# Kernel optimization log

Measured on AMD Instinct MI355X. Metric: run time of the kernel, lower is better.

## Reference

```python
import jax, jax.numpy as jnp
import numpy as np

H = 8          # num_heads
DM = 128       # dmodel
BN_EPS = 1e-5


def _linear(x, w, b):
    # w stored as [in, out]
    return x @ w + b


def _relu_mha(q, k, v, qw, qb, kw, kb, vw, vb, ow, ob, mask):
    """TemMulHeadAtte: ReLU on projected Q/K/V, masked softmax, ReLU out-proj.
    q,k: [B,N,T,2*DM]; v: [B,N,T,DM]; mask: broadcastable to [B,N,H,T,T] or None."""
    B, N, T, _ = q.shape
    Q = jax.nn.relu(_linear(q, qw, qb)).reshape(B, N, T, H, -1)  # e = 2*DM/H
    K = jax.nn.relu(_linear(k, kw, kb)).reshape(B, N, T, H, -1)
    V = jax.nn.relu(_linear(v, vw, vb)).reshape(B, N, T, H, -1)  # d = DM/H
    scale = 1.0 / np.sqrt(Q.shape[-1]).astype(np.float32)
    scores = jnp.einsum('bnthe,bnshe->bnhts', Q, K)
    if mask is not None:
        scores = jnp.where(mask, -jnp.inf, scores)
    attn = jax.nn.softmax(scale * scores, axis=-1)  # dropout p=0 -> identity
    out = jnp.einsum('bnhts,bnshd->bnthd', attn, V).reshape(B, N, T, -1)
    return jax.nn.relu(_linear(out, ow, ob))


def setup_inputs() -> dict:
    key = jax.random.key(0)
    ks = iter(jax.random.split(key, 32))
    B, N, T = 16, 207, 24
    def w(shape, scale=0.05):
        return (jax.random.normal(next(ks), shape, dtype=jnp.float32) * scale)
    inp = {
        'x': w((B, N, T, DM), 1.0),
        'hidden': w((B, N, T, DM), 1.0),
        'tXin': w((B, N, T, DM), 1.0),
    }
    dk = 2 * DM // H * H   # 256
    dv = DM // H * H       # 128
    for pre in ('s', 't'):  # space / temporal attention params
        inp[pre + 'q_w'] = w((2 * DM, dk)); inp[pre + 'q_b'] = w((dk,))
        inp[pre + 'k_w'] = w((2 * DM, dk)); inp[pre + 'k_b'] = w((dk,))
        inp[pre + 'v_w'] = w((DM, dv));     inp[pre + 'v_b'] = w((dv,))
        inp[pre + 'o_w'] = w((dv, DM));     inp[pre + 'o_b'] = w((DM,))
    inp['gate_w'] = w((2 * DM, DM)); inp['gate_b'] = w((DM,))
    inp['bn_gamma'] = jnp.ones((DM,), jnp.float32)
    inp['bn_beta'] = jnp.zeros((DM,), jnp.float32)
    return inp


def reference(x, hidden, tXin,
              sq_w, sq_b, sk_w, sk_b, sv_w, sv_b, so_w, so_b,
              tq_w, tq_b, tk_w, tk_b, tv_w, tv_b, to_w, to_b,
              gate_w, gate_b, bn_gamma, bn_beta):
    B, N, T, E = hidden.shape
    ht = jnp.concatenate([hidden, tXin], axis=3)  # [B,N,T,2*DM]
    # spatial attention: attend over nodes (N<->T permute)
    sqk = ht.transpose(0, 2, 1, 3)        # [B,T,N,2*DM]
    sval = hidden.transpose(0, 2, 1, 3)   # [B,T,N,DM]
    spaceOut = _relu_mha(sqk, sqk, sval, sq_w, sq_b, sk_w, sk_b, sv_w, sv_b,
                         so_w, so_b, None).transpose(0, 2, 1, 3)  # [B,N,T,DM]
    # temporal attention with causal (strict upper-tri) mask
    mask = jnp.triu(jnp.ones((T, T), dtype=bool), 1)[None, None, None]
    tempOut = _relu_mha(ht, ht, hidden, tq_w, tq_b, tk_w, tk_b, tv_w, tv_b,
                        to_w, to_b, mask)  # [B,N,T,DM]
    # gate + BatchNorm2d over channel dim (training-mode batch stats, biased var)
    gi = _linear(jnp.concatenate([spaceOut, tempOut], axis=3), gate_w, gate_b)
    mean = gi.mean(axis=(0, 1, 2))
    var = gi.var(axis=(0, 1, 2))
    z = jax.nn.sigmoid((gi - mean) * jax.lax.rsqrt(var + BN_EPS) * bn_gamma + bn_beta)
    return z * spaceOut + (1.0 - z) * tempOut
```

## Files before the change

kernel.cpp:

```cpp
#include <hip/hip_runtime.h>
#include <hip/hip_bf16.h>

typedef __bf16 bf16;
typedef __bf16 bf16x8 __attribute__((ext_vector_type(8)));
typedef float f32x4 __attribute__((ext_vector_type(4)));

#define MTOT 79488
#define NDIM 207
#define TDIM 24

#define EXP2F(x) __builtin_amdgcn_exp2f(x)

__global__ void detect_dtype(const void* __restrict__ hidden, int* __restrict__ flag)
{
    __shared__ int cnt;
    if (threadIdx.x == 0) cnt = 0;
    __syncthreads();
    const bf16* h = (const bf16*)hidden;
    int local = 0;
    for (int i = threadIdx.x; i < 4096; i += 256) {
        float v = (float)h[i];
        if (!(fabsf(v) < 1e6f)) local++;
    }
    atomicAdd(&cnt, local);
    __syncthreads();
    if (threadIdx.x == 0) *flag = (cnt > 8) ? 1 : 0;
}

__device__ inline float ld_ext(const void* p, int idx, int isF32)
{
    return isF32 ? ((const float*)p)[idx] : (float)((const bf16*)p)[idx];
}

__global__ __launch_bounds__(256) void cvt_inputs(
    const void* __restrict__ hidden, const void* __restrict__ tXin,
    bf16* __restrict__ hb, bf16* __restrict__ tb, const int* __restrict__ dtf)
{
    const int isF32 = *dtf;
    const void* src = blockIdx.y ? tXin : hidden;
    bf16* dst = blockIdx.y ? tb : hb;
    const size_t e8 = ((size_t)blockIdx.x * 256 + threadIdx.x) * 8;
    bf16x8 v;
    if (isF32) {
        f32x4 lo = *(const f32x4*)((const float*)src + e8);
        f32x4 hi = *(const f32x4*)((const float*)src + e8 + 4);
        v[0]=(bf16)lo[0]; v[1]=(bf16)lo[1]; v[2]=(bf16)lo[2]; v[3]=(bf16)lo[3];
        v[4]=(bf16)hi[0]; v[5]=(bf16)hi[1]; v[6]=(bf16)hi[2]; v[7]=(bf16)hi[3];
    } else {
        v = *(const bf16x8*)((const bf16*)src + e8);
    }
    *(bf16x8*)(dst + e8) = v;
}

__global__ __launch_bounds__(256) void prep_weights(
    const void* __restrict__ sq, const void* __restrict__ sk, const void* __restrict__ sv,
    const void* __restrict__ so, const void* __restrict__ tq, const void* __restrict__ tk,
    const void* __restrict__ tv, const void* __restrict__ to_, const void* __restrict__ gw,
    const void* __restrict__ sqb, const void* __restrict__ skb, const void* __restrict__ svb,
    const void* __restrict__ sob, const void* __restrict__ tqb, const void* __restrict__ tkb,
    const void* __restrict__ tvb, const void* __restrict__ tob, const void* __restrict__ gb,
    bf16* __restrict__ wdst, bf16* __restrict__ bdst, const int* __restrict__ dtf)
{
    const int isF32 = *dtf;
    if (blockIdx.x == 1536) {
        for (int j = threadIdx.x; j < 1664; j += 256) {
            const void* src; int i2;
            if      (j < 256)  { src = sqb; i2 = j; }
            else if (j < 512)  { src = skb; i2 = j - 256; }
            else if (j < 640)  { src = svb; i2 = j - 512; }
            else if (j < 896)  { src = tqb; i2 = j - 640; }
            else if (j < 1152) { src = tkb; i2 = j - 896; }
            else if (j < 1280) { src = tvb; i2 = j - 1152; }
            else if (j < 1408) { src = sob; i2 = j - 1280; }
            else if (j < 1536) { src = tob; i2 = j - 1408; }
            else               { src = gb;  i2 = j - 1536; }
            bdst[j] = (bf16)ld_ext(src, i2, isF32);
        }
        return;
    }
    const int e = blockIdx.x * 256 + threadIdx.x;
    float v;
    if (e < 327680) {
        int br = (e >= 163840);
        int e2 = e - br * 163840;
        int n = e2 >> 8, k = e2 & 255;
        const void* qw = br ? tq : sq;
        const void* kw = br ? tk : sk;
        const void* vw = br ? tv : sv;
        if      (n < 256) v = ld_ext(qw, k * 256 + n, isF32);
        else if (n < 512) v = ld_ext(kw, k * 256 + (n - 256), isF32);
        else              v = (k < 128) ? ld_ext(vw, k * 128 + (n - 512), isF32) : 0.f;
    } else if (e < 360448) {
        int br = (e >= 344064);
        int e2 = e - 327680 - br * 16384;
        int n = e2 >> 7, k = e2 & 127;
        v = ld_ext(br ? to_ : so, k * 128 + n, isF32);
    } else {
        int e2 = e - 360448;
        int n = e2 >> 8, k = e2 & 255;
        v = ld_ext(gw, k * 128 + n, isF32);
    }
    wdst[e] = (bf16)v;
}

__global__ __launch_bounds__(256) void gemm_bt(
    const void* __restrict__ A0v, const void* __restrict__ A1v,
    const bf16* __restrict__ Bt, const bf16* __restrict__ bias,
    bf16* __restrict__ C, int Nout, int Ktot, int doRelu, int aExt,
    const int* __restrict__ dtf, int permMode, float* __restrict__ stats, int ntx)
{
    const int aF32 = aExt & *dtf;
    __shared__ bf16 smem[2 * 128 * 72];
    bf16* As = smem;
    bf16* Bs = smem + 128 * 72;
    __shared__ float lsum[128], lsq[128];
    const int tid  = threadIdx.x;
    const int wid  = tid >> 6, lane = tid & 63;
    const int wm   = (wid >> 1) * 64, wn = (wid & 1) * 64;
    const int quad = lane >> 4, l16 = lane & 15;

    int m0, n0;
    {
        const int nwg = (int)gridDim.x;
        const int lid = (int)blockIdx.x;
        const int q = nwg >> 3, r = nwg & 7;
        const int xcd = lid & 7, idx = lid >> 3;
        const int nid = (xcd < r ? xcd * (q + 1) : r * (q + 1) + (xcd - r) * q) + idx;
        m0 = (nid / ntx) * 128;
        n0 = (nid % ntx) * 128;
    }

    const int lrow = tid >> 3;
    const int lcol = (tid & 7) * 8;

    bf16x8 av[4], bv[4];
    auto loadTiles = [&](int k0) {
        const void* Ap = (k0 < 128) ? A0v : A1v;
        const int koff = (k0 < 128) ? k0 : k0 - 128;
        #pragma unroll
        for (int p = 0; p < 4; ++p) {
            int r = lrow + p * 32;
            if (aF32) {
                const float* Af = (const float*)Ap;
                f32x4 lo = *(const f32x4*)(Af + (size_t)(m0 + r) * 128 + koff + lcol);
                f32x4 hi = *(const f32x4*)(Af + (size_t)(m0 + r) * 128 + koff + lcol + 4);
                bf16x8 t;
                t[0]=(bf16)lo[0]; t[1]=(bf16)lo[1]; t[2]=(bf16)lo[2]; t[3]=(bf16)lo[3];
                t[4]=(bf16)hi[0]; t[5]=(bf16)hi[1]; t[6]=(bf16)hi[2]; t[7]=(bf16)hi[3];
                av[p] = t;
            } else {
                av[p] = *(const bf16x8*)((const bf16*)Ap + (size_t)(m0 + r) * 128 + koff + lcol);
            }
            bv[p] = *(const bf16x8*)(Bt + (size_t)(n0 + r) * Ktot + k0 + lcol);
        }
    };

    loadTiles(0);
    f32x4 acc[4][4] = {};

    for (int k0 = 0; k0 < Ktot; k0 += 64) {
        #pragma unroll
        for (int p = 0; p < 4; ++p) {
            int r = lrow + p * 32;
            *(bf16x8*)&As[r * 72 + lcol] = av[p];
            *(bf16x8*)&Bs[r * 72 + lcol] = bv[p];
        }
        __syncthreads();
        if (k0 + 64 < Ktot) loadTiles(k0 + 64);
        #pragma unroll
        for (int kk = 0; kk < 64; kk += 32) {
            bf16x8 af[4], bfr[4];
            #pragma unroll
            for (int i = 0; i < 4; ++i)
                af[i] = *(const bf16x8*)&As[(wm + i * 16 + l16) * 72 + kk + quad * 8];
            #pragma unroll
            for (int j = 0; j < 4; ++j)
                bfr[j] = *(const bf16x8*)&Bs[(wn + j * 16 + l16) * 72 + kk + quad * 8];
            #pragma unroll
            for (int i = 0; i < 4; ++i)
                #pragma unroll
                for (int j = 0; j < 4; ++j)
                    acc[i][j] = __builtin_amdgcn_mfma_f32_16x16x32_bf16(
                        af[i], bfr[j], acc[i][j], 0, 0, 0);
        }
        __syncthreads();
    }

    if (stats) {
        if (tid < 128) { lsum[tid] = 0.f; lsq[tid] = 0.f; }
        __syncthreads();
    }
    #pragma unroll
    for (int j = 0; j < 4; ++j) {
        int col = n0 + wn + j * 16 + l16;
        float bv2 = (float)bias[col];
        float ps = 0.f, psq = 0.f;
        #pragma unroll
        for (int i = 0; i < 4; ++i) {
            #pragma unroll
            for (int r = 0; r < 4; ++r) {
                float v = acc[i][j][r] + bv2;
                if (doRelu) v = fmaxf(v, 0.f);
                if (stats) { ps += v; psq += v * v; }
                acc[i][j][r] = v;
            }
        }
        if (stats) {
            atomicAdd(&lsum[col & 127], ps);
            atomicAdd(&lsq[col & 127], psq);
        }
    }

    bf16* Cs = smem;
    #pragma unroll
    for (int j = 0; j < 4; ++j)
        #pragma unroll
        for (int i = 0; i < 4; ++i)
            #pragma unroll
            for (int r = 0; r < 4; ++r)
                Cs[(wm + i * 16 + quad * 4 + r) * 132 + wn + j * 16 + l16]
                    = (bf16)acc[i][j][r];
    __syncthreads();

    if (stats && tid < 128) {
        atomicAdd(&stats[tid], lsum[tid]);
        atomicAdd(&stats[128 + tid], lsq[tid]);
    }

    const int srow = tid >> 4, scol = (tid & 15) * 8;
    #pragma unroll
    for (int pass = 0; pass < 8; ++pass) {
        int rl = pass * 16 + srow;
        int m = m0 + rl;
        int o;
        if (permMode == 1) {
            int t = m % 24, bn = m / 24;
            int n = bn % 207, b = bn / 207;
            o = (b * 24 + t) * 207 + n;
        } else if (permMode == 2) {
            int n = m % 207, bt = m / 207;
            int t = bt % 24, b = bt / 24;
            o = (b * 207 + n) * 24 + t;
        } else {
            o = m;
        }
        bf16x8 v = *(const bf16x8*)&Cs[rl * 132 + scol];
        *(bf16x8*)&C[(size_t)o * Nout + n0 + scol] = v;
    }
}

__global__ __launch_bounds__(256) void attn_spatial_mfma(
    const bf16* __restrict__ QKV, bf16* __restrict__ O)
{
    const int hh = blockIdx.x, t = blockIdx.y, b = blockIdx.z;
    __shared__ bf16 Ks[208 * 40];
    __shared__ bf16 Vt[16 * 232];
    __shared__ bf16 Pl[4][2][16 * 40];
    const int tid = threadIdx.x;
    const int wave = tid >> 6, lane = tid & 63;
    const int quad = lane >> 4, l16 = lane & 15;
    const size_t R = (size_t)(b * TDIM + t) * NDIM;

    for (int idx = tid; idx < 832; idx += 256) {
        int n = idx >> 2, seg = (idx & 3) * 8;
        bf16x8 v8 = {};
        if (n < NDIM)
            v8 = *(const bf16x8*)(QKV + (R + n) * 640 + 256 + hh * 32 + seg);
        *(bf16x8*)&Ks[n * 40 + seg] = v8;
    }
    for (int idx = tid; idx < 448; idx += 256) {
        int s = idx >> 1, half = (idx & 1) * 8;
        bf16x8 v8 = {};
        if (s < NDIM)
            v8 = *(const bf16x8*)(QKV + (R + s) * 640 + 512 + hh * 16 + half);
        #pragma unroll
        for (int j = 0; j < 8; ++j)
            Vt[(half + j) * 232 + s] = v8[j];
    }
    __syncthreads();

    const float k2 = 0.25506538410868237f;

    for (int qt = wave; qt < 13; qt += 4) {
        const int q0 = qt * 16;
        int qrow = q0 + l16; if (qrow >= NDIM) qrow = NDIM - 1;
        bf16x8 qfrag = *(const bf16x8*)(QKV + (R + qrow) * 640 + hh * 32 + quad * 8);
        f32x4 s[13];
        #pragma unroll
        for (int c = 0; c < 13; ++c) {
            bf16x8 kf = *(const bf16x8*)&Ks[(c * 16 + l16) * 40 + quad * 8];
            f32x4 z = {};
            s[c] = __builtin_amdgcn_mfma_f32_16x16x32_bf16(qfrag, kf, z, 0, 0, 0);
        }
        float linv[4];
        #pragma unroll
        for (int r = 0; r < 4; ++r) {
            float sum = 0.f;
            #pragma unroll
            for (int c = 0; c < 13; ++c) {
                float p = EXP2F(s[c][r] * k2);
                if (c == 12 && l16 == 15) p = 0.f;
                s[c][r] = p;
                sum += p;
            }
            sum += __shfl_xor(sum, 1);
            sum += __shfl_xor(sum, 2);
            sum += __shfl_xor(sum, 4);
            sum += __shfl_xor(sum, 8);
            linv[r] = __builtin_amdgcn_rcpf(sum);
        }
        f32x4 oacc = {};
        #pragma unroll
        for (int sc = 0; sc < 7; ++sc) {
            bf16* pb = &Pl[wave][sc & 1][0];
            #pragma unroll
            for (int r = 0; r < 4; ++r) {
                float p1 = 0.f;
                if (sc < 6) p1 = s[2 * sc + 1][r];
                pb[(quad * 4 + r) * 40 + l16]      = (bf16)s[2 * sc][r];
                pb[(quad * 4 + r) * 40 + 16 + l16] = (bf16)p1;
            }
            bf16x8 pf = *(const bf16x8*)&pb[l16 * 40 + quad * 8];
            bf16x8 vf = *(const bf16x8*)&Vt[l16 * 232 + sc * 32 + quad * 8];
            oacc = __builtin_amdgcn_mfma_f32_16x16x32_bf16(pf, vf, oacc, 0, 0, 0);
        }
        #pragma unroll
        for (int r = 0; r < 4; ++r) {
            int row = q0 + quad * 4 + r;
            if (row < NDIM)
                O[(R + row) * 128 + hh * 16 + l16] = (bf16)(oacc[r] * linv[r]);
        }
    }
}

__global__ __launch_bounds__(256) void attn_temporal_mfma(
    const bf16* __restrict__ QKV, bf16* __restrict__ O)
{
    const size_t m0 = (size_t)blockIdx.x * TDIM;
    __shared__ bf16 Khs[8 * 32 * 40];
    __shared__ bf16 Vts[8 * 16 * 40];
    __shared__ bf16 Pl[4][2][16 * 40];
    const int tid = threadIdx.x;
    const int wave = tid >> 6, lane = tid & 63;
    const int quad = lane >> 4, l16 = lane & 15;
    const int STR = 640;

    for (int idx = tid; idx < 32 * 32; idx += 256) {
        int row = idx >> 5, seg = idx & 31;
        int h = seg >> 2, j = (seg & 3) * 8;
        bf16x8 v8 = {};
        if (row < TDIM)
            v8 = *(const bf16x8*)(QKV + (m0 + row) * STR + 256 + h * 32 + j);
        *(bf16x8*)&Khs[h * 1280 + row * 40 + j] = v8;
    }
    for (int idx = tid; idx < 32 * 128; idx += 256) {
        int s = idx >> 7, c = idx & 127;
        int h = c >> 4, d = c & 15;
        bf16 v = (bf16)0.f;
        if (s < TDIM) v = QKV[(m0 + s) * STR + 512 + h * 16 + d];
        Vts[h * 640 + d * 40 + s] = v;
    }
    __syncthreads();

    const float k2 = 0.25506538410868237f;

    #pragma unroll
    for (int hi = 0; hi < 2; ++hi) {
        const int h = wave * 2 + hi;
        #pragma unroll
        for (int qt = 0; qt < 2; ++qt) {
            int qrow = qt * 16 + l16; if (qrow >= TDIM) qrow = TDIM - 1;
            bf16x8 qfrag = *(const bf16x8*)(QKV + (m0 + qrow) * STR + h * 32 + quad * 8);
            bf16x8 kf0 = *(const bf16x8*)&Khs[h * 1280 + l16 * 40 + quad * 8];
            bf16x8 kf1 = *(const bf16x8*)&Khs[h * 1280 + (16 + l16) * 40 + quad * 8];
            f32x4 z = {};
            f32x4 s0 = __builtin_amdgcn_mfma_f32_16x16x32_bf16(qfrag, kf0, z, 0, 0, 0);
            f32x4 s1 = __builtin_amdgcn_mfma_f32_16x16x32_bf16(qfrag, kf1, z, 0, 0, 0);
            bf16* pb = &Pl[wave][qt][0];
            float linv[4];
            #pragma unroll
            for (int r = 0; r < 4; ++r) {
                int q = qt * 16 + quad * 4 + r;
                float p0 = (l16 <= q)      ? EXP2F(s0[r] * k2) : 0.f;
                float p1 = (16 + l16 <= q) ? EXP2F(s1[r] * k2) : 0.f;
                float sum = p0 + p1;
                sum += __shfl_xor(sum, 1);
                sum += __shfl_xor(sum, 2);
                sum += __shfl_xor(sum, 4);
                sum += __shfl_xor(sum, 8);
                linv[r] = __builtin_amdgcn_rcpf(sum);
                pb[(quad * 4 + r) * 40 + l16]      = (bf16)p0;
                pb[(quad * 4 + r) * 40 + 16 + l16] = (bf16)p1;
            }
            bf16x8 pf = *(const bf16x8*)&pb[l16 * 40 + quad * 8];
            bf16x8 vf = *(const bf16x8*)&Vts[h * 640 + l16 * 40 + quad * 8];
            f32x4 oacc = __builtin_amdgcn_mfma_f32_16x16x32_bf16(pf, vf, z, 0, 0, 0);
            #pragma unroll
            for (int r = 0; r < 4; ++r) {
                int row = qt * 16 + quad * 4 + r;
                if (row < TDIM)
                    O[(m0 + row) * 128 + h * 16 + l16] = (bf16)(oacc[r] * linv[r]);
            }
        }
    }
}

__global__ __launch_bounds__(256) void bn_final(
    const bf16* __restrict__ gi, const bf16* __restrict__ sp, const bf16* __restrict__ tp,
    const void* __restrict__ gammav, const void* __restrict__ betav,
    const float* __restrict__ stats, void* __restrict__ outv,
    const int* __restrict__ dtf)
{
    const int isF32 = *dtf;
    const size_t base = ((size_t)blockIdx.x * 256 + threadIdx.x) * 8;
    const int c0 = (int)(base & 127);
    const float invM = 1.f / (float)MTOT;
    bf16x8 g8 = *(const bf16x8*)(gi + base);
    bf16x8 s8 = *(const bf16x8*)(sp + base);
    bf16x8 t8 = *(const bf16x8*)(tp + base);
    float res[8];
    #pragma unroll
    for (int j = 0; j < 8; ++j) {
        int c = c0 + j;
        float mean = stats[c] * invM;
        float var  = stats[128 + c] * invM - mean * mean;
        float gam = ld_ext(gammav, c, isF32);
        float bet = ld_ext(betav, c, isF32);
        float g = (float)g8[j];
        float zn = (g - mean) * rsqrtf(var + 1e-5f) * gam + bet;
        float z = 1.f / (1.f + EXP2F(zn * -1.4426950408889634f));
        float sv = (float)s8[j], tv = (float)t8[j];
        res[j] = z * sv + (1.f - z) * tv;
    }
    if (isF32) {
        float* op = (float*)outv + base;
        f32x4 lo = {res[0], res[1], res[2], res[3]};
        f32x4 hi = {res[4], res[5], res[6], res[7]};
        *(f32x4*)op = lo;
        *(f32x4*)(op + 4) = hi;
    } else {
        bf16x8 o8;
        #pragma unroll
        for (int j = 0; j < 8; ++j) o8[j] = (bf16)res[j];
        *(bf16x8*)((bf16*)outv + base) = o8;
    }
}

extern "C" void kernel_launch(void* const* d_in, const int* in_sizes, int n_in,
                              void* d_out, int out_size, void* d_ws, size_t ws_size,
                              hipStream_t stream)
{
    const void* hidden = d_in[1];
    const void* tXin   = d_in[2];
    const void* sq_w = d_in[3];  const void* sq_b = d_in[4];
    const void* sk_w = d_in[5];  const void* sk_b = d_in[6];
    const void* sv_w = d_in[7];  const void* sv_b = d_in[8];
    const void* so_w = d_in[9];  const void* so_b = d_in[10];
    const void* tq_w = d_in[11]; const void* tq_b = d_in[12];
    const void* tk_w = d_in[13]; const void* tk_b = d_in[14];
    const void* tv_w = d_in[15]; const void* tv_b = d_in[16];
    const void* to_w = d_in[17]; const void* to_b = d_in[18];
    const void* gate_w = d_in[19]; const void* gate_b = d_in[20];
    const void* gamma  = d_in[21]; const void* beta   = d_in[22];

    char* ws = (char*)d_ws;
    float* stats = (float*)ws;
    int*  dtf    = (int*)(ws + 1024);
    bf16* bB     = (bf16*)(ws + 2048);
    bf16* wT     = (bf16*)(ws + 8192);
    bf16* spaceO = (bf16*)(ws + 794624);
    bf16* attnO  = (bf16*)(ws + 21143552);
    bf16* QKV    = (bf16*)(ws + 41492480);
    bf16* hb     = (bf16*)(ws + 143237120);
    bf16* tb     = (bf16*)(ws + 163586048);
    bf16* tempO  = attnO;
    bf16* gi     = QKV;

    const int wsBig = (ws_size >= 184000000ull);

    bf16* sW  = wT;            bf16* tW  = wT + 163840;
    bf16* soT = wT + 327680;   bf16* toT = wT + 344064;
    bf16* gwT = wT + 360448;

    (void)hipMemsetAsync(stats, 0, 1024, stream);
    detect_dtype<<<1, 256, 0, stream>>>(hidden, dtf);
    prep_weights<<<dim3(1537), 256, 0, stream>>>(
        sq_w, sk_w, sv_w, so_w, tq_w, tk_w, tv_w, to_w, gate_w,
        sq_b, sk_b, sv_b, so_b, tq_b, tk_b, tv_b, to_b, gate_b,
        wT, bB, dtf);
    if (wsBig)
        cvt_inputs<<<dim3(4968, 2), 256, 0, stream>>>(hidden, tXin, hb, tb, dtf);

    const void* A0 = wsBig ? (const void*)hb : hidden;
    const void* A1 = wsBig ? (const void*)tb : tXin;
    const int aExt = wsBig ? 0 : 1;

    gemm_bt<<<dim3(3105), 256, 0, stream>>>(A0, A1, sW, bB, QKV, 640, 256, 1, aExt, dtf, 1, nullptr, 5);
    attn_spatial_mfma<<<dim3(8, TDIM, 16), 256, 0, stream>>>(QKV, attnO);
    gemm_bt<<<dim3(621), 256, 0, stream>>>(attnO, nullptr, soT, bB + 1280, spaceO, 128, 128, 1, 0, dtf, 2, nullptr, 1);

    gemm_bt<<<dim3(3105), 256, 0, stream>>>(A0, A1, tW, bB + 640, QKV, 640, 256, 1, aExt, dtf, 0, nullptr, 5);
    attn_temporal_mfma<<<dim3(16 * NDIM), 256, 0, stream>>>(QKV, attnO);
    gemm_bt<<<dim3(621), 256, 0, stream>>>(attnO, nullptr, toT, bB + 1408, tempO, 128, 128, 1, 0, dtf, 0, nullptr, 1);

    gemm_bt<<<dim3(621), 256, 0, stream>>>(spaceO, tempO, gwT, bB + 1536, gi, 128, 256, 0, 0, dtf, 0, stats, 1);
    bn_final<<<dim3(4968), 256, 0, stream>>>(gi, spaceO, tempO, gamma, beta, stats, d_out, dtf);
}
```

Baseline: 494.0 us.

## Merge spatial/temporal projection GEMMs into single launches and drop input conversion pass

Reworks the launch plan based on workspace size. With a large workspace, the spatial and temporal QKV projections run as one GEMM launch, and both output projections run as one launch with dual outputs. The separate bf16 input conversion kernel and the memset are removed; the GEMM now reads f32 inputs directly and detect_dtype zeroes the stats. The attention kernels also write P with packed bf16x2 stores and use an interleaved V key layout to match. This cuts launch count and an extra full pass over the inputs, at the cost of more workspace, extra per-block branching, and converting A on the fly inside the GEMM.

```diff
diff --git a/kernel.cpp b/kernel.cpp
--- a/kernel.cpp
+++ b/kernel.cpp
@@ -2,6 +2,7 @@
 #include <hip/hip_bf16.h>
 
 typedef __bf16 bf16;
+typedef __bf16 bf16x2 __attribute__((ext_vector_type(2)));
 typedef __bf16 bf16x8 __attribute__((ext_vector_type(8)));
 typedef float f32x4 __attribute__((ext_vector_type(4)));
 
@@ -11,10 +12,12 @@
 
 #define EXP2F(x) __builtin_amdgcn_exp2f(x)
 
-__global__ void detect_dtype(const void* __restrict__ hidden, int* __restrict__ flag)
+__global__ void detect_dtype(const void* __restrict__ hidden, int* __restrict__ flag,
+                             float* __restrict__ stats)
 {
     __shared__ int cnt;
     if (threadIdx.x == 0) cnt = 0;
+    stats[threadIdx.x] = 0.f;
     __syncthreads();
     const bf16* h = (const bf16*)hidden;
     int local = 0;
@@ -30,26 +33,6 @@
 __device__ inline float ld_ext(const void* p, int idx, int isF32)
 {
     return isF32 ? ((const float*)p)[idx] : (float)((const bf16*)p)[idx];
-}
-
-__global__ __launch_bounds__(256) void cvt_inputs(
-    const void* __restrict__ hidden, const void* __restrict__ tXin,
-    bf16* __restrict__ hb, bf16* __restrict__ tb, const int* __restrict__ dtf)
-{
-    const int isF32 = *dtf;
-    const void* src = blockIdx.y ? tXin : hidden;
-    bf16* dst = blockIdx.y ? tb : hb;
-    const size_t e8 = ((size_t)blockIdx.x * 256 + threadIdx.x) * 8;
-    bf16x8 v;
-    if (isF32) {
-        f32x4 lo = *(const f32x4*)((const float*)src + e8);
-        f32x4 hi = *(const f32x4*)((const float*)src + e8 + 4);
-        v[0]=(bf16)lo[0]; v[1]=(bf16)lo[1]; v[2]=(bf16)lo[2]; v[3]=(bf16)lo[3];
-        v[4]=(bf16)hi[0]; v[5]=(bf16)hi[1]; v[6]=(bf16)hi[2]; v[7]=(bf16)hi[3];
-    } else {
-        v = *(const bf16x8*)((const bf16*)src + e8);
-    }
-    *(bf16x8*)(dst + e8) = v;
 }
 
 __global__ __launch_bounds__(256) void prep_weights(
@@ -105,9 +88,12 @@
 
 __global__ __launch_bounds__(256) void gemm_bt(
     const void* __restrict__ A0v, const void* __restrict__ A1v,
+    const void* __restrict__ A0bv,
     const bf16* __restrict__ Bt, const bf16* __restrict__ bias,
-    bf16* __restrict__ C, int Nout, int Ktot, int doRelu, int aExt,
-    const int* __restrict__ dtf, int permMode, float* __restrict__ stats, int ntx)
+    bf16* __restrict__ Ca, bf16* __restrict__ Cb,
+    int Nout, int Ktot, int doRelu, int aExt,
+    const int* __restrict__ dtf, int pmA, int pmB,
+    float* __restrict__ stats, int ntx, int nSplit, int mSplit)
 {
     const int aF32 = aExt & *dtf;
     __shared__ bf16 smem[2 * 128 * 72];
@@ -119,23 +105,27 @@
     const int wm   = (wid >> 1) * 64, wn = (wid & 1) * 64;
     const int quad = lane >> 4, l16 = lane & 15;
 
-    int m0, n0;
+    int panel, n0;
     {
         const int nwg = (int)gridDim.x;
         const int lid = (int)blockIdx.x;
         const int q = nwg >> 3, r = nwg & 7;
         const int xcd = lid & 7, idx = lid >> 3;
         const int nid = (xcd < r ? xcd * (q + 1) : r * (q + 1) + (xcd - r) * q) + idx;
-        m0 = (nid / ntx) * 128;
+        panel = nid / ntx;
         n0 = (nid % ntx) * 128;
     }
+    const int gB = (panel >= mSplit);
+    if (gB) panel -= mSplit;
+    const int m0 = panel * 128;
+    const int brOff = gB ? Nout : 0;
 
     const int lrow = tid >> 3;
     const int lcol = (tid & 7) * 8;
 
     bf16x8 av[4], bv[4];
     auto loadTiles = [&](int k0) {
-        const void* Ap = (k0 < 128) ? A0v : A1v;
+        const void* Ap = gB ? A0bv : ((k0 < 128) ? A0v : A1v);
         const int koff = (k0 < 128) ? k0 : k0 - 128;
         #pragma unroll
         for (int p = 0; p < 4; ++p) {
@@ -151,7 +141,7 @@
             } else {
                 av[p] = *(const bf16x8*)((const bf16*)Ap + (size_t)(m0 + r) * 128 + koff + lcol);
             }
-            bv[p] = *(const bf16x8*)(Bt + (size_t)(n0 + r) * Ktot + k0 + lcol);
+            bv[p] = *(const bf16x8*)(Bt + (size_t)(n0 + brOff + r) * Ktot + k0 + lcol);
         }
     };
 
@@ -186,13 +176,18 @@
         __syncthreads();
     }
 
+    bf16* Cp; int pm; int c0;
+    if (nSplit && n0 >= nSplit) { Cp = Cb; pm = pmB; c0 = n0 - nSplit; }
+    else if (gB)                { Cp = Cb; pm = pmB; c0 = n0; }
+    else                        { Cp = Ca; pm = pmA; c0 = n0; }
+
     if (stats) {
         if (tid < 128) { lsum[tid] = 0.f; lsq[tid] = 0.f; }
         __syncthreads();
     }
     #pragma unroll
     for (int j = 0; j < 4; ++j) {
-        int col = n0 + wn + j * 16 + l16;
+        int col = n0 + brOff + wn + j * 16 + l16;
         float bv2 = (float)bias[col];
         float ps = 0.f, psq = 0.f;
         #pragma unroll
@@ -233,11 +228,11 @@
         int rl = pass * 16 + srow;
         int m = m0 + rl;
         int o;
-        if (permMode == 1) {
+        if (pm == 1) {
             int t = m % 24, bn = m / 24;
             int n = bn % 207, b = bn / 207;
             o = (b * 24 + t) * 207 + n;
-        } else if (permMode == 2) {
+        } else if (pm == 2) {
             int n = m % 207, bt = m / 207;
             int t = bt % 24, b = bt / 24;
             o = (b * 207 + n) * 24 + t;
@@ -245,8 +240,13 @@
             o = m;
         }
         bf16x8 v = *(const bf16x8*)&Cs[rl * 132 + scol];
-        *(bf16x8*)&C[(size_t)o * Nout + n0 + scol] = v;
-    }
+        *(bf16x8*)&Cp[(size_t)o * Nout + c0 + scol] = v;
+    }
+}
+
+__device__ inline int kpos(int i)
+{
+    return (i < 16) ? (i << 1) : (((i - 16) << 1) | 1);
 }
 
 __global__ __launch_bounds__(256) void attn_spatial_mfma(
@@ -273,9 +273,10 @@
         bf16x8 v8 = {};
         if (s < NDIM)
             v8 = *(const bf16x8*)(QKV + (R + s) * 640 + 512 + hh * 16 + half);
+        int spos = (s & ~31) + kpos(s & 31);
         #pragma unroll
         for (int j = 0; j < 8; ++j)
-            Vt[(half + j) * 232 + s] = v8[j];
+            Vt[(half + j) * 232 + spos] = v8[j];
     }
     __syncthreads();
 
@@ -315,10 +316,10 @@
             bf16* pb = &Pl[wave][sc & 1][0];
             #pragma unroll
             for (int r = 0; r < 4; ++r) {
-                float p1 = 0.f;
-                if (sc < 6) p1 = s[2 * sc + 1][r];
-                pb[(quad * 4 + r) * 40 + l16]      = (bf16)s[2 * sc][r];
-                pb[(quad * 4 + r) * 40 + 16 + l16] = (bf16)p1;
+                bf16x2 pk;
+                pk[0] = (bf16)s[2 * sc][r];
+                pk[1] = (sc < 6) ? (bf16)s[2 * sc + 1][r] : (bf16)0.f;
+                *(bf16x2*)&pb[(quad * 4 + r) * 40 + 2 * l16] = pk;
             }
             bf16x8 pf = *(const bf16x8*)&pb[l16 * 40 + quad * 8];
             bf16x8 vf = *(const bf16x8*)&Vt[l16 * 232 + sc * 32 + quad * 8];
@@ -358,7 +359,7 @@
         int h = c >> 4, d = c & 15;
         bf16 v = (bf16)0.f;
         if (s < TDIM) v = QKV[(m0 + s) * STR + 512 + h * 16 + d];
-        Vts[h * 640 + d * 40 + s] = v;
+        Vts[h * 640 + d * 40 + kpos(s)] = v;
     }
     __syncthreads();
 
@@ -389,8 +390,8 @@
                 sum += __shfl_xor(sum, 4);
                 sum += __shfl_xor(sum, 8);
                 linv[r] = __builtin_amdgcn_rcpf(sum);
-                pb[(quad * 4 + r) * 40 + l16]      = (bf16)p0;
-                pb[(quad * 4 + r) * 40 + 16 + l16] = (bf16)p1;
+                bf16x2 pk; pk[0] = (bf16)p0; pk[1] = (bf16)p1;
+                *(bf16x2*)&pb[(quad * 4 + r) * 40 + 2 * l16] = pk;
             }
             bf16x8 pf = *(const bf16x8*)&pb[l16 * 40 + quad * 8];
             bf16x8 vf = *(const bf16x8*)&Vts[h * 640 + l16 * 40 + quad * 8];
@@ -469,40 +470,61 @@
     bf16* bB     = (bf16*)(ws + 2048);
     bf16* wT     = (bf16*)(ws + 8192);
     bf16* spaceO = (bf16*)(ws + 794624);
-    bf16* attnO  = (bf16*)(ws + 21143552);
-    bf16* QKV    = (bf16*)(ws + 41492480);
-    bf16* hb     = (bf16*)(ws + 143237120);
-    bf16* tb     = (bf16*)(ws + 163586048);
-    bf16* tempO  = attnO;
-    bf16* gi     = QKV;
-
-    const int wsBig = (ws_size >= 184000000ull);
-
+    bf16* attnOs = (bf16*)(ws + 21143552);
+    bf16* QKVs   = (bf16*)(ws + 41492480);
+    bf16* attnOt = (bf16*)(ws + 143237120);
+    bf16* QKVt   = (bf16*)(ws + 163586048);
+    bf16* gi     = QKVs;
+
+    const int tier = (ws_size >= 265330688ull) ? 2
+                   : (ws_size >= 163586048ull) ? 1 : 0;
+    if (tier == 0) attnOt = attnOs;
+    bf16* tempO = attnOt;
     bf16* sW  = wT;            bf16* tW  = wT + 163840;
-    bf16* soT = wT + 327680;   bf16* toT = wT + 344064;
+    bf16* soT = wT + 327680;
     bf16* gwT = wT + 360448;
-
-    (void)hipMemsetAsync(stats, 0, 1024, stream);
-    detect_dtype<<<1, 256, 0, stream>>>(hidden, dtf);
+    const int BIG = 1 << 28;
+
+    detect_dtype<<<1, 256, 0, stream>>>(hidden, dtf, stats);
     prep_weights<<<dim3(1537), 256, 0, stream>>>(
         sq_w, sk_w, sv_w, so_w, tq_w, tk_w, tv_w, to_w, gate_w,
         sq_b, sk_b, sv_b, so_b, tq_b, tk_b, tv_b, to_b, gate_b,
         wT, bB, dtf);
-    if (wsBig)
-        cvt_inputs<<<dim3(4968, 2), 256, 0, stream>>>(hidden, tXin, hb, tb, dtf);
-
-    const void* A0 = wsBig ? (const void*)hb : hidden;
-    const void* A1 = wsBig ? (const void*)tb : tXin;
-    const int aExt = wsBig ? 0 : 1;
-
-    gemm_bt<<<dim3(3105), 256, 0, stream>>>(A0, A1, sW, bB, QKV, 640, 256, 1, aExt, dtf, 1, nullptr, 5);
-    attn_spatial_mfma<<<dim3(8, TDIM, 16), 256, 0, stream>>>(QKV, attnO);
-    gemm_bt<<<dim3(621), 256, 0, stream>>>(attnO, nullptr, soT, bB + 1280, spaceO, 128, 128, 1, 0, dtf, 2, nullptr, 1);
-
-    gemm_bt<<<dim3(3105), 256, 0, stream>>>(A0, A1, tW, bB + 640, QKV, 640, 256, 1, aExt, dtf, 0, nullptr, 5);
-    attn_temporal_mfma<<<dim3(16 * NDIM), 256, 0, stream>>>(QKV, attnO);
-    gemm_bt<<<dim3(621), 256, 0, stream>>>(attnO, nullptr, toT, bB + 1408, tempO, 128, 128, 1, 0, dtf, 0, nullptr, 1);
-
-    gemm_bt<<<dim3(621), 256, 0, stream>>>(spaceO, tempO, gwT, bB + 1536, gi, 128, 256, 0, 0, dtf, 0, stats, 1);
+
+    if (tier == 2) {
+        gemm_bt<<<dim3(6210), 256, 0, stream>>>(
+            hidden, tXin, nullptr, wT, bB, QKVs, QKVt,
+            640, 256, 1, 1, dtf, 1, 0, nullptr, 10, 640, BIG);
+        attn_spatial_mfma<<<dim3(8, TDIM, 16), 256, 0, stream>>>(QKVs, attnOs);
+        attn_temporal_mfma<<<dim3(16 * NDIM), 256, 0, stream>>>(QKVt, attnOt);
+    } else {
+        gemm_bt<<<dim3(3105), 256, 0, stream>>>(
+            hidden, tXin, nullptr, sW, bB, QKVs, nullptr,
+            640, 256, 1, 1, dtf, 1, 0, nullptr, 5, 0, BIG);
+        attn_spatial_mfma<<<dim3(8, TDIM, 16), 256, 0, stream>>>(QKVs, attnOs);
+        if (tier == 0) {
+            gemm_bt<<<dim3(621), 256, 0, stream>>>(
+                attnOs, nullptr, nullptr, soT, bB + 1280, spaceO, nullptr,
+                128, 128, 1, 0, dtf, 2, 0, nullptr, 1, 0, BIG);
+        }
+        gemm_bt<<<dim3(3105), 256, 0, stream>>>(
+            hidden, tXin, nullptr, tW, bB + 640, QKVs, nullptr,
+            640, 256, 1, 1, dtf, 0, 0, nullptr, 5, 0, BIG);
+        attn_temporal_mfma<<<dim3(16 * NDIM), 256, 0, stream>>>(QKVs, attnOt);
+    }
+
+    if (tier >= 1) {
+        gemm_bt<<<dim3(1242), 256, 0, stream>>>(
+            attnOs, nullptr, attnOt, soT, bB + 1280, spaceO, tempO,
+            128, 128, 1, 0, dtf, 2, 0, nullptr, 1, 0, 621);
+    } else {
+        gemm_bt<<<dim3(621), 256, 0, stream>>>(
+            attnOt, nullptr, nullptr, soT + 16384, bB + 1408, tempO, nullptr,
+            128, 128, 1, 0, dtf, 0, 0, nullptr, 1, 0, BIG);
+    }
+
+    gemm_bt<<<dim3(621), 256, 0, stream>>>(
+        spaceO, tempO, nullptr, gwT, bB + 1536, gi, nullptr,
+        128, 256, 0, 0, dtf, 0, 0, stats, 1, 0, BIG);
     bn_final<<<dim3(4968), 256, 0, stream>>>(gi, spaceO, tempO, gamma, beta, stats, d_out, dtf);
 }
```

After: 543.1 us. +9.9%, slower.
